# Performance work log

Measured on AMD Instinct MI355X. Metric: run time of the kernel, lower is better.

Reference implementation:

```python
import jax, jax.numpy as jnp
import numpy as np


def setup_inputs() -> dict:
    key = jax.random.key(0)
    k1, k2, k3 = jax.random.split(key, 3)
    B, D, R, O = 8192, 2048, 16, 64
    # small init scale so the 2048-step matrix chain product stays numerically sane
    inputs = jax.random.normal(k1, (B, D), dtype=jnp.float32) * 0.05
    # cores near identity (glorot-scale perturbation) to avoid chain blow-up/collapse
    cores = jnp.eye(R, dtype=jnp.float32)[None] + jax.random.normal(k2, (D, R, R), dtype=jnp.float32) * (1.0 / R)
    projection = jax.random.normal(k3, (R, O), dtype=jnp.float32) * (1.0 / np.sqrt(R))
    bias = jnp.zeros((O,), dtype=jnp.float32)
    return {"inputs": inputs, "cores": cores, "projection": projection, "bias": bias}


def reference(inputs, cores, projection, bias):
    # inputs: (B, D); cores: (D, R, R); projection: (R, O); bias: (O,)
    B = inputs.shape[0]
    R = cores.shape[-1]
    boundary0 = jnp.ones((B, R), dtype=inputs.dtype)  # MPS boundary vector

    x_t = inputs.T  # (D, B) so scan iterates over features

    def step(boundary, xs):
        core, x = xs  # core: (R, R), x: (B,)
        # boundary <- (boundary @ core) scaled by the feature value (A^i[x_i])
        boundary = jnp.matmul(boundary, core) * x[:, None]
        return boundary, None

    boundary, _ = jax.lax.scan(step, boundary0, (cores, x_t))
    out = jnp.matmul(boundary, projection) + bias  # (B, O)
    return out
```

## Files before the change

### kernel.cpp

```cpp
#include <hip/hip_runtime.h>
#include <math.h>


#define DFEAT 2048
#define R 16
#define NR2 256
#define OUTD 64
#define CHUNK 64
#define NCHUNK (DFEAT / CHUNK)
#define MAGIC 0x7E57C0DE

__global__ __launch_bounds__(256) void mps_chain(const float* __restrict__ cores,
                                                 const float* __restrict__ proj,
                                                 float* __restrict__ partials,
                                                 int* __restrict__ flags,
                                                 float* __restrict__ pE) {
    __shared__ __align__(16) float Cs[CHUNK][R][R];
    __shared__ float A[2][R][R];
    __shared__ __align__(16) float Pt[NCHUNK][R][R];
    const int tid = threadIdx.x;
    const int i = tid >> 4, j = tid & 15;
    const size_t d0 = (size_t)blockIdx.x * CHUNK;

    const float4* g4 = (const float4*)(cores + d0 * NR2);
    float4* s4 = (float4*)&Cs[0][0][0];
#pragma unroll
    for (int q = 0; q < 16; ++q)
        s4[q * 256 + tid] = g4[q * 256 + tid];

    A[0][i][j] = (i == j) ? 1.f : 0.f;
    __syncthreads();

    int cur = 0;
    for (int t = 0; t < CHUNK; ++t) {
        float acc = 0.f;
#pragma unroll
        for (int k = 0; k < R; ++k)
            acc = fmaf(A[cur][i][k], Cs[t][k][j], acc);
        A[cur ^ 1][i][j] = acc;
        cur ^= 1;
        __syncthreads();
    }
    const float v = A[cur][i][j];

    if (blockIdx.x != 0) {
        partials[blockIdx.x * NR2 + tid] = v;
        __syncthreads();
        if (tid == 0)
            __hip_atomic_store(&flags[blockIdx.x], MAGIC,
                               __ATOMIC_RELEASE, __HIP_MEMORY_SCOPE_AGENT);
        return;
    }

    Pt[0][j][i] = v;

    {
        const int f = 1 + (tid % (NCHUNK - 1));
        while (__hip_atomic_load(&flags[f], __ATOMIC_ACQUIRE,
                                 __HIP_MEMORY_SCOPE_AGENT) != MAGIC) { }
    }
    __syncthreads();

#pragma unroll
    for (int q = 0; q < 8; ++q) {
        const int idx = q * 256 + tid;
        if (idx < (NCHUNK - 1) * 64) {
            float4 p4 = ((const float4*)(partials + NR2))[idx];
            const int flat = idx * 4;
            const int gg = (flat >> 8) + 1;
            const int e = flat & 255;
            const int k = e >> 4, j0 = e & 15;
            Pt[gg][j0 + 0][k] = p4.x;
            Pt[gg][j0 + 1][k] = p4.y;
            Pt[gg][j0 + 2][k] = p4.z;
            Pt[gg][j0 + 3][k] = p4.w;
        }
    }
    __syncthreads();

    if (tid < 64) {
        const int jj = tid & 15, q = tid >> 4;
        float w = 1.f;
        int E = 0;
        for (int gg = 0; gg < NCHUNK; ++gg) {
            const float4 pr = *(const float4*)&Pt[gg][jj][4 * q];
            float s;
            s = __shfl(w, 4 * q + 0) * pr.x;
            s = fmaf(__shfl(w, 4 * q + 1), pr.y, s);
            s = fmaf(__shfl(w, 4 * q + 2), pr.z, s);
            s = fmaf(__shfl(w, 4 * q + 3), pr.w, s);
            s += __shfl_xor(s, 16);
            s += __shfl_xor(s, 32);
            w = s;
            if ((gg & 7) == 7) {
                float m = fabsf(w);
#pragma unroll
                for (int off = 1; off <= 8; off <<= 1)
                    m = fmaxf(m, __shfl_xor(m, off));
                if (m > 0.f) {
                    int e = 0;
                    (void)frexpf(m, &e);
                    w = ldexpf(w, -e);
                    E += e;
                }
            }
        }
        float p = 0.f;
#pragma unroll
        for (int k = 0; k < R; ++k)
            p = fmaf(__shfl(w, k), proj[k * OUTD + tid], p);
        pE[tid] = p;
        if (tid == 0) ((int*)pE)[OUTD] = E;
    }
}

__global__ __launch_bounds__(256) void mps_rows(const float* __restrict__ x,
                                                const float* __restrict__ pE,
                                                const float* __restrict__ bias,
                                                float* __restrict__ out,
                                                int B) {
    const int gtid = blockIdx.x * 256 + threadIdx.x;
    const int row  = gtid >> 6;
    const int lane = threadIdx.x & 63;
    if (row >= B) return;

    const float4* xr = (const float4*)(x + (size_t)row * DFEAT);
    float prod = 1.f;
#pragma unroll
    for (int it = 0; it < DFEAT / (64 * 4); ++it) {
        float4 v = xr[it * 64 + lane];
        prod *= (v.x * v.y) * (v.z * v.w);
    }
#pragma unroll
    for (int off = 32; off > 0; off >>= 1)
        prod *= __shfl_xor(prod, off);

    const float pv = pE[lane];
    const int   E  = ((const int*)pE)[OUTD];
    out[(size_t)row * OUTD + lane] = ldexpf(pv * prod, E) + bias[lane];
}

extern "C" void kernel_launch(void* const* d_in, const int* in_sizes, int n_in,
                              void* d_out, int out_size, void* d_ws, size_t ws_size,
                              hipStream_t stream) {
    const float* inputs = (const float*)d_in[0];
    const float* cores  = (const float*)d_in[1];
    const float* proj   = (const float*)d_in[2];
    const float* bias   = (const float*)d_in[3];
    float* out = (float*)d_out;

    float* partials = (float*)d_ws;
    float* pE    = partials + NCHUNK * NR2;
    int*   flags = (int*)(pE + 68);

    const int B = in_sizes[0] / DFEAT;

    mps_chain<<<NCHUNK, 256, 0, stream>>>(cores, proj, partials, flags, pE);
    mps_rows<<<(B * 64 + 255) / 256, 256, 0, stream>>>(inputs, pE, bias, out, B);
}
```

Before: 113.5 us.

## Split chunk chain across four waves to remove per-step block barriers

Each block's 64-core chain product is now split into four wave-local 16-core sub-chains. Each wave computes its sub-chain with register-blocked float4 row products and needs no block-wide barrier between steps. Wave 0 then multiplies the four partial products together. This replaces 64 __syncthreads per block with two, at the cost of an extra short combine phase in which only one wave works.

```diff
diff --git a/kernel.cpp b/kernel.cpp
--- a/kernel.cpp
+++ b/kernel.cpp
@@ -10,38 +10,71 @@
 #define NCHUNK (DFEAT / CHUNK)
 #define MAGIC 0x7E57C0DE
 
+__device__ __forceinline__ float4 rowmul(const float* Arow, const float* B,
+                                         int c0) {
+    float4 acc = {0.f, 0.f, 0.f, 0.f};
+    const float4* a4 = (const float4*)Arow;
+#pragma unroll
+    for (int kk = 0; kk < 4; ++kk) {
+        const float4 av = a4[kk];
+        const float4 b0 = *(const float4*)&B[(4 * kk + 0) * 16 + c0];
+        const float4 b1 = *(const float4*)&B[(4 * kk + 1) * 16 + c0];
+        const float4 b2 = *(const float4*)&B[(4 * kk + 2) * 16 + c0];
+        const float4 b3 = *(const float4*)&B[(4 * kk + 3) * 16 + c0];
+        acc.x = fmaf(av.x, b0.x, fmaf(av.y, b1.x, fmaf(av.z, b2.x, fmaf(av.w, b3.x, acc.x))));
+        acc.y = fmaf(av.x, b0.y, fmaf(av.y, b1.y, fmaf(av.z, b2.y, fmaf(av.w, b3.y, acc.y))));
+        acc.z = fmaf(av.x, b0.z, fmaf(av.y, b1.z, fmaf(av.z, b2.z, fmaf(av.w, b3.z, acc.z))));
+        acc.w = fmaf(av.x, b0.w, fmaf(av.y, b1.w, fmaf(av.z, b2.w, fmaf(av.w, b3.w, acc.w))));
+    }
+    return acc;
+}
+
 __global__ __launch_bounds__(256) void mps_chain(const float* __restrict__ cores,
                                                  const float* __restrict__ proj,
                                                  float* __restrict__ partials,
                                                  int* __restrict__ flags,
                                                  float* __restrict__ pE) {
-    __shared__ __align__(16) float Cs[CHUNK][R][R];
-    __shared__ float A[2][R][R];
-    __shared__ __align__(16) float Pt[NCHUNK][R][R];
-    const int tid = threadIdx.x;
-    const int i = tid >> 4, j = tid & 15;
+    __shared__ __align__(16) float Cs[CHUNK * NR2];
+    __shared__ __align__(16) float Aw[4][2][NR2];
+    __shared__ __align__(16) float F[2][NR2];
+    __shared__ __align__(16) float Pt[NCHUNK * NR2];
+    const int tid  = threadIdx.x;
+    const int wave = tid >> 6, lane = tid & 63;
+    const int ri = lane >> 2;
+    const int c0 = (lane & 3) << 2;
     const size_t d0 = (size_t)blockIdx.x * CHUNK;
 
     const float4* g4 = (const float4*)(cores + d0 * NR2);
-    float4* s4 = (float4*)&Cs[0][0][0];
+    float4* s4 = (float4*)&Cs[0];
 #pragma unroll
     for (int q = 0; q < 16; ++q)
         s4[q * 256 + tid] = g4[q * 256 + tid];
-
-    A[0][i][j] = (i == j) ? 1.f : 0.f;
     __syncthreads();
 
+    *(float4*)&Aw[wave][0][ri * 16 + c0] =
+        *(const float4*)&Cs[(16 * wave) * NR2 + ri * 16 + c0];
     int cur = 0;
-    for (int t = 0; t < CHUNK; ++t) {
-        float acc = 0.f;
-#pragma unroll
-        for (int k = 0; k < R; ++k)
-            acc = fmaf(A[cur][i][k], Cs[t][k][j], acc);
-        A[cur ^ 1][i][j] = acc;
+    for (int t = 1; t < 16; ++t) {
+        float4 r = rowmul(&Aw[wave][cur][ri * 16],
+                          &Cs[(16 * wave + t) * NR2], c0);
+        *(float4*)&Aw[wave][cur ^ 1][ri * 16 + c0] = r;
         cur ^= 1;
-        __syncthreads();
     }
-    const float v = A[cur][i][j];
+    __syncthreads();
+
+    if (wave == 0) {
+        *(float4*)&F[0][ri * 16 + c0] =
+            *(const float4*)&Aw[0][1][ri * 16 + c0];
+        int cc = 0;
+        for (int w = 1; w < 4; ++w) {
+            float4 r = rowmul(&F[cc][ri * 16], &Aw[w][1][0], c0);
+            *(float4*)&F[cc ^ 1][ri * 16 + c0] = r;
+            cc ^= 1;
+        }
+    }
+    __syncthreads();
+    const int i = tid >> 4, j = tid & 15;
+    const float v = F[1][tid];
 
     if (blockIdx.x != 0) {
         partials[blockIdx.x * NR2 + tid] = v;
@@ -52,7 +85,7 @@
         return;
     }
 
-    Pt[0][j][i] = v;
+    Pt[0 * 256 + j * 16 + i] = v;
 
     {
         const int f = 1 + (tid % (NCHUNK - 1));
@@ -70,10 +103,10 @@
             const int gg = (flat >> 8) + 1;
             const int e = flat & 255;
             const int k = e >> 4, j0 = e & 15;
-            Pt[gg][j0 + 0][k] = p4.x;
-            Pt[gg][j0 + 1][k] = p4.y;
-            Pt[gg][j0 + 2][k] = p4.z;
-            Pt[gg][j0 + 3][k] = p4.w;
+            Pt[gg * 256 + (j0 + 0) * 16 + k] = p4.x;
+            Pt[gg * 256 + (j0 + 1) * 16 + k] = p4.y;
+            Pt[gg * 256 + (j0 + 2) * 16 + k] = p4.z;
+            Pt[gg * 256 + (j0 + 3) * 16 + k] = p4.w;
         }
     }
     __syncthreads();
@@ -83,7 +116,7 @@
         float w = 1.f;
         int E = 0;
         for (int gg = 0; gg < NCHUNK; ++gg) {
-            const float4 pr = *(const float4*)&Pt[gg][jj][4 * q];
+            const float4 pr = *(const float4*)&Pt[gg * 256 + jj * 16 + 4 * q];
             float s;
             s = __shfl(w, 4 * q + 0) * pr.x;
             s = fmaf(__shfl(w, 4 * q + 1), pr.y, s);
```

Result: faster. 106.1 us (-6.5%).
